# Kernel optimization log

Measured on AMD Instinct MI355X. Metric: run time of the kernel, lower is better.

Reference implementation:

```python
import jax, jax.numpy as jnp
import numpy as np

E, N, D, H = 500000, 100000, 128, 128
LN_EPS = 1e-5


def setup_inputs() -> dict:
    key = jax.random.key(0)
    ks = jax.random.split(key, 8)
    efeat = jax.random.normal(ks[0], (E, D), dtype=jnp.float32)
    nfeat = jax.random.normal(ks[1], (N, D), dtype=jnp.float32)
    src = jax.random.randint(ks[2], (E,), 0, N, dtype=jnp.int64)
    dst = jax.random.randint(ks[3], (E,), 0, N, dtype=jnp.int64)
    dim_cat = 2 * D + D  # 2*input_dim_nodes + input_dim_edges = 384
    w1 = jax.random.normal(ks[4], (dim_cat, H), dtype=jnp.float32) / np.sqrt(dim_cat)
    b1 = jnp.zeros((H,), dtype=jnp.float32)
    w2 = jax.random.normal(ks[5], (H, D), dtype=jnp.float32) / np.sqrt(H)
    b2 = jnp.zeros((D,), dtype=jnp.float32)
    gamma = jnp.ones((D,), dtype=jnp.float32)
    beta = jnp.zeros((D,), dtype=jnp.float32)
    return {"efeat": efeat, "nfeat": nfeat, "src": src, "dst": dst,
            "w1": w1, "b1": b1, "w2": w2, "b2": b2, "gamma": gamma, "beta": beta}


def reference(efeat, nfeat, src, dst, w1, b1, w2, b2, gamma, beta):
    # gather per-edge src/dst node features and concat with edge features: [E, 2D+D]
    cat_feat = jnp.concatenate([efeat, nfeat[src], nfeat[dst]], axis=-1)
    # MeshGraphMLP with hidden_layers=1: Linear -> SiLU -> Linear -> LayerNorm
    h = jax.nn.silu(cat_feat @ w1 + b1)          # [E, H]
    y = h @ w2 + b2                               # [E, D]
    mu = jnp.mean(y, axis=-1, keepdims=True)
    var = jnp.mean((y - mu) ** 2, axis=-1, keepdims=True)
    y = (y - mu) * jax.lax.rsqrt(var + LN_EPS) * gamma + beta
    efeat_new = y + efeat                         # residual add
    return (efeat_new, nfeat)
```

## Files before the change

### kernel.cpp

```cpp
#include <hip/hip_runtime.h>

#define E_CONST 500000
#define N_CONST 100000

typedef __attribute__((ext_vector_type(8))) short bf16x8;
typedef __attribute__((ext_vector_type(4))) float f32x4;
typedef __attribute__((ext_vector_type(4))) unsigned u32x4;

__global__ __launch_bounds__(256) void prep_weights(const float* __restrict__ w1,
                                                    const float* __restrict__ w2,
                                                    short* __restrict__ ws) {
    int idx  = blockIdx.x * 256 + threadIdx.x;
    int frag = idx >> 9;
    int r    = idx & 511;
    int lane = r >> 3, j = r & 7;
    const float* w;
    int fi;
    if (frag < 96) { w = w1; fi = frag; }
    else           { w = w2; fi = frag - 96; }
    int kk = fi >> 3, nn = fi & 7;
    int k = kk * 32 + (lane >> 4) * 8 + j;
    int n = nn * 16 + (lane & 15);
    unsigned u = __float_as_uint(w[k * 128 + n]);
    u = u + 0x7FFFu + ((u >> 16) & 1u);
    ws[idx] = (short)(u >> 16);
}

__global__ __launch_bounds__(256) void copy_nfeat(const float* __restrict__ nfeat,
                                                  float* __restrict__ out) {
    size_t idx = (size_t)(blockIdx.x * 256 + threadIdx.x) * 4;
    *(f32x4*)(out + idx) = *(const f32x4*)(nfeat + idx);
}

__device__ __forceinline__ unsigned pack_bf16_trunc(float lo, float hi) {
    return __builtin_amdgcn_perm(__float_as_uint(hi), __float_as_uint(lo), 0x07060302u);
}

__global__ __launch_bounds__(256, 2) void edge_mlp(
    const float* __restrict__ efeat, const float* __restrict__ nfeat,
    const int* __restrict__ src, const int* __restrict__ dst,
    const short* __restrict__ wsw,
    const float* __restrict__ b1, const float* __restrict__ b2,
    const float* __restrict__ gamma, const float* __restrict__ beta,
    float* __restrict__ out) {

    __shared__ short hs[64 * 136];
    __shared__ float ys[64 * 132];
    __shared__ float mu_s[64];
    __shared__ float rs_s[64];

    const int tid   = threadIdx.x;
    const int lane  = tid & 63;
    const int nw    = tid >> 6;
    const int l15   = lane & 15;
    const int quad  = lane >> 4;
    const int eBase = blockIdx.x * 64;

    bf16x8 b1f[2][12];
    bf16x8 b2f[2][4];
#pragma unroll
    for (int t = 0; t < 2; ++t) {
        int nn = nw * 2 + t;
#pragma unroll
        for (int kk = 0; kk < 12; ++kk)
            b1f[t][kk] = *(const bf16x8*)(wsw + ((kk * 8 + nn) * 64 + lane) * 8);
#pragma unroll
        for (int kk = 0; kk < 4; ++kk)
            b2f[t][kk] = *(const bf16x8*)(wsw + 49152 + ((kk * 8 + nn) * 64 + lane) * 8);
    }
    const float bb1[2] = { b1[nw * 32 + l15], b1[nw * 32 + 16 + l15] };
    const float bb2[2] = { b2[nw * 32 + l15], b2[nw * 32 + 16 + l15] };

#pragma unroll 1
    for (int mt = 0; mt < 4; ++mt) {
        int e = eBase + mt * 16 + l15;
        if (e >= E_CONST) e = E_CONST - 1;
        int s = src[e], d = dst[e];
        const float* pe = efeat + (size_t)e * 128 + quad * 8;
        const float* ps = nfeat + (size_t)s * 128 + quad * 8;
        const float* pd = nfeat + (size_t)d * 128 + quad * 8;

        f32x4 acc0 = {0.f, 0.f, 0.f, 0.f}, acc1 = {0.f, 0.f, 0.f, 0.f};
#pragma unroll
        for (int kk = 0; kk < 12; ++kk) {
            const float* p = (kk < 4) ? (pe + kk * 32)
                           : (kk < 8) ? (ps + (kk - 4) * 32)
                                      : (pd + (kk - 8) * 32);
            f32x4 f0 = *(const f32x4*)p;
            f32x4 f1 = *(const f32x4*)(p + 4);
            u32x4 pk;
            pk.x = pack_bf16_trunc(f0.x, f0.y);
            pk.y = pack_bf16_trunc(f0.z, f0.w);
            pk.z = pack_bf16_trunc(f1.x, f1.y);
            pk.w = pack_bf16_trunc(f1.z, f1.w);
            bf16x8 a = __builtin_bit_cast(bf16x8, pk);
            acc0 = __builtin_amdgcn_mfma_f32_16x16x32_bf16(a, b1f[0][kk], acc0, 0, 0, 0);
            acc1 = __builtin_amdgcn_mfma_f32_16x16x32_bf16(a, b1f[1][kk], acc1, 0, 0, 0);
        }
#pragma unroll
        for (int t = 0; t < 2; ++t) {
            f32x4 acc = (t == 0) ? acc0 : acc1;
            int col = nw * 32 + t * 16 + l15;
#pragma unroll
            for (int i = 0; i < 4; ++i) {
                float x  = acc[i] + bb1[t];
                float sg = __builtin_amdgcn_rcpf(1.0f + __expf(-x));
                float h  = x * sg;
                int row  = mt * 16 + quad * 4 + i;
                unsigned u = __float_as_uint(h);
                u = u + 0x7FFFu + ((u >> 16) & 1u);
                hs[row * 136 + col] = (short)(u >> 16);
            }
        }
    }
    __syncthreads();

#pragma unroll 1
    for (int mt = 0; mt < 4; ++mt) {
        int arow = mt * 16 + l15;
        f32x4 acc0 = {0.f, 0.f, 0.f, 0.f}, acc1 = {0.f, 0.f, 0.f, 0.f};
#pragma unroll
        for (int kk = 0; kk < 4; ++kk) {
            bf16x8 a = *(const bf16x8*)(hs + arow * 136 + kk * 32 + quad * 8);
            acc0 = __builtin_amdgcn_mfma_f32_16x16x32_bf16(a, b2f[0][kk], acc0, 0, 0, 0);
            acc1 = __builtin_amdgcn_mfma_f32_16x16x32_bf16(a, b2f[1][kk], acc1, 0, 0, 0);
        }
#pragma unroll
        for (int t = 0; t < 2; ++t) {
            f32x4 acc = (t == 0) ? acc0 : acc1;
            int col = nw * 32 + t * 16 + l15;
#pragma unroll
            for (int i = 0; i < 4; ++i)
                ys[(mt * 16 + quad * 4 + i) * 132 + col] = acc[i] + bb2[t];
        }
    }
    __syncthreads();

    {
        int row = tid >> 2;
        int part = tid & 3;
        const float* yr = ys + row * 132 + part * 32;
        float sum = 0.f, sq = 0.f;
#pragma unroll
        for (int k = 0; k < 8; ++k) {
            f32x4 v = *(const f32x4*)(yr + k * 4);
            sum += v.x + v.y + v.z + v.w;
            sq  += v.x * v.x + v.y * v.y + v.z * v.z + v.w * v.w;
        }
        sum += __shfl_xor(sum, 1); sq += __shfl_xor(sq, 1);
        sum += __shfl_xor(sum, 2); sq += __shfl_xor(sq, 2);
        if (part == 0) {
            float mu  = sum * (1.0f / 128.0f);
            float var = sq * (1.0f / 128.0f) - mu * mu;
            mu_s[row] = mu;
            rs_s[row] = __builtin_amdgcn_rsqf(var + 1e-5f);
        }
    }
    __syncthreads();

    {
        int c4 = tid & 31;
        f32x4 g4  = *(const f32x4*)(gamma + c4 * 4);
        f32x4 bt4 = *(const f32x4*)(beta  + c4 * 4);
#pragma unroll 1
        for (int it = 0; it < 8; ++it) {
            int row = it * 8 + (tid >> 5);
            int e = eBase + row;
            if (e < E_CONST) {
                float mu = mu_s[row], rs = rs_s[row];
                f32x4 y  = *(const f32x4*)(ys + row * 132 + c4 * 4);
                f32x4 ef = *(const f32x4*)(efeat + (size_t)e * 128 + c4 * 4);
                f32x4 o;
                o.x = (y.x - mu) * rs * g4.x + bt4.x + ef.x;
                o.y = (y.y - mu) * rs * g4.y + bt4.y + ef.y;
                o.z = (y.z - mu) * rs * g4.z + bt4.z + ef.z;
                o.w = (y.w - mu) * rs * g4.w + bt4.w + ef.w;
                *(f32x4*)(out + (size_t)e * 128 + c4 * 4) = o;
            }
        }
    }
}

extern "C" void kernel_launch(void* const* d_in, const int* in_sizes, int n_in,
                              void* d_out, int out_size, void* d_ws, size_t ws_size,
                              hipStream_t stream) {
    const float* efeat = (const float*)d_in[0];
    const float* nfeat = (const float*)d_in[1];
    const int*   src   = (const int*)d_in[2];
    const int*   dst   = (const int*)d_in[3];
    const float* w1    = (const float*)d_in[4];
    const float* b1    = (const float*)d_in[5];
    const float* w2    = (const float*)d_in[6];
    const float* b2    = (const float*)d_in[7];
    const float* gamma = (const float*)d_in[8];
    const float* beta  = (const float*)d_in[9];
    float* out = (float*)d_out;
    short* wsw = (short*)d_ws;

    hipLaunchKernelGGL(prep_weights, dim3(256), dim3(256), 0, stream, w1, w2, wsw);
    hipLaunchKernelGGL(copy_nfeat, dim3(12500), dim3(256), 0, stream,
                       nfeat, out + (size_t)E_CONST * 128);
    hipLaunchKernelGGL(edge_mlp, dim3((E_CONST + 63) / 64), dim3(256), 0, stream,
                       efeat, nfeat, src, dst, wsw, b1, b2, gamma, beta, out);
}
```

Measured before the change: 844.9 us.

## Raise occupancy by streaming weights, reusing LDS for bf16 y, batching loads

```diff
diff --git a/kernel.cpp b/kernel.cpp
--- a/kernel.cpp
+++ b/kernel.cpp
@@ -6,6 +6,8 @@
 typedef __attribute__((ext_vector_type(8))) short bf16x8;
 typedef __attribute__((ext_vector_type(4))) float f32x4;
 typedef __attribute__((ext_vector_type(4))) unsigned u32x4;
+typedef __attribute__((ext_vector_type(8))) unsigned short u16x8;
+typedef __attribute__((ext_vector_type(4))) unsigned short u16x4;
 
 __global__ __launch_bounds__(256) void prep_weights(const float* __restrict__ w1,
                                                     const float* __restrict__ w2,
@@ -26,17 +28,17 @@
     ws[idx] = (short)(u >> 16);
 }
 
-__global__ __launch_bounds__(256) void copy_nfeat(const float* __restrict__ nfeat,
-                                                  float* __restrict__ out) {
-    size_t idx = (size_t)(blockIdx.x * 256 + threadIdx.x) * 4;
-    *(f32x4*)(out + idx) = *(const f32x4*)(nfeat + idx);
-}
-
 __device__ __forceinline__ unsigned pack_bf16_trunc(float lo, float hi) {
     return __builtin_amdgcn_perm(__float_as_uint(hi), __float_as_uint(lo), 0x07060302u);
 }
 
-__global__ __launch_bounds__(256, 2) void edge_mlp(
+__device__ __forceinline__ unsigned short to_bf16(float x) {
+    unsigned u = __float_as_uint(x);
+    u = u + 0x7FFFu + ((u >> 16) & 1u);
+    return (unsigned short)(u >> 16);
+}
+
+__global__ __launch_bounds__(256, 4) void edge_mlp(
     const float* __restrict__ efeat, const float* __restrict__ nfeat,
     const int* __restrict__ src, const int* __restrict__ dst,
     const short* __restrict__ wsw,
@@ -45,7 +47,6 @@
     float* __restrict__ out) {
 
     __shared__ short hs[64 * 136];
-    __shared__ float ys[64 * 132];
     __shared__ float mu_s[64];
     __shared__ float rs_s[64];
 
@@ -56,18 +57,11 @@
     const int quad  = lane >> 4;
     const int eBase = blockIdx.x * 64;
 
-    bf16x8 b1f[2][12];
-    bf16x8 b2f[2][4];
-#pragma unroll
-    for (int t = 0; t < 2; ++t) {
-        int nn = nw * 2 + t;
-#pragma unroll
-        for (int kk = 0; kk < 12; ++kk)
-            b1f[t][kk] = *(const bf16x8*)(wsw + ((kk * 8 + nn) * 64 + lane) * 8);
-#pragma unroll
-        for (int kk = 0; kk < 4; ++kk)
-            b2f[t][kk] = *(const bf16x8*)(wsw + 49152 + ((kk * 8 + nn) * 64 + lane) * 8);
-    }
+    int ee = eBase + lane;
+    if (ee >= E_CONST) ee = E_CONST - 1;
+    const int vsrc = src[ee];
+    const int vdst = dst[ee];
+
     const float bb1[2] = { b1[nw * 32 + l15], b1[nw * 32 + 16 + l15] };
     const float bb2[2] = { b2[nw * 32 + l15], b2[nw * 32 + 16 + l15] };
 
@@ -75,27 +69,35 @@
     for (int mt = 0; mt < 4; ++mt) {
         int e = eBase + mt * 16 + l15;
         if (e >= E_CONST) e = E_CONST - 1;
-        int s = src[e], d = dst[e];
+        int s = __shfl(vsrc, mt * 16 + l15);
+        int d = __shfl(vdst, mt * 16 + l15);
         const float* pe = efeat + (size_t)e * 128 + quad * 8;
         const float* ps = nfeat + (size_t)s * 128 + quad * 8;
         const float* pd = nfeat + (size_t)d * 128 + quad * 8;
 
-        f32x4 acc0 = {0.f, 0.f, 0.f, 0.f}, acc1 = {0.f, 0.f, 0.f, 0.f};
+        f32x4 fa[12], fb[12];
 #pragma unroll
         for (int kk = 0; kk < 12; ++kk) {
             const float* p = (kk < 4) ? (pe + kk * 32)
                            : (kk < 8) ? (ps + (kk - 4) * 32)
                                       : (pd + (kk - 8) * 32);
-            f32x4 f0 = *(const f32x4*)p;
-            f32x4 f1 = *(const f32x4*)(p + 4);
+            fa[kk] = *(const f32x4*)p;
+            fb[kk] = *(const f32x4*)(p + 4);
+        }
+
+        f32x4 acc0 = {0.f, 0.f, 0.f, 0.f}, acc1 = {0.f, 0.f, 0.f, 0.f};
+#pragma unroll
+        for (int kk = 0; kk < 12; ++kk) {
             u32x4 pk;
-            pk.x = pack_bf16_trunc(f0.x, f0.y);
-            pk.y = pack_bf16_trunc(f0.z, f0.w);
-            pk.z = pack_bf16_trunc(f1.x, f1.y);
-            pk.w = pack_bf16_trunc(f1.z, f1.w);
+            pk.x = pack_bf16_trunc(fa[kk].x, fa[kk].y);
+            pk.y = pack_bf16_trunc(fa[kk].z, fa[kk].w);
+            pk.z = pack_bf16_trunc(fb[kk].x, fb[kk].y);
+            pk.w = pack_bf16_trunc(fb[kk].z, fb[kk].w);
             bf16x8 a = __builtin_bit_cast(bf16x8, pk);
-            acc0 = __builtin_amdgcn_mfma_f32_16x16x32_bf16(a, b1f[0][kk], acc0, 0, 0, 0);
-            acc1 = __builtin_amdgcn_mfma_f32_16x16x32_bf16(a, b1f[1][kk], acc1, 0, 0, 0);
+            bf16x8 w0 = *(const bf16x8*)(wsw + ((kk * 8 + nw * 2 + 0) * 64 + lane) * 8);
+            bf16x8 w1f = *(const bf16x8*)(wsw + ((kk * 8 + nw * 2 + 1) * 64 + lane) * 8);
+            acc0 = __builtin_amdgcn_mfma_f32_16x16x32_bf16(a, w0, acc0, 0, 0, 0);
+            acc1 = __builtin_amdgcn_mfma_f32_16x16x32_bf16(a, w1f, acc1, 0, 0, 0);
         }
 #pragma unroll
         for (int t = 0; t < 2; ++t) {
@@ -107,14 +109,13 @@
                 float sg = __builtin_amdgcn_rcpf(1.0f + __expf(-x));
                 float h  = x * sg;
                 int row  = mt * 16 + quad * 4 + i;
-                unsigned u = __float_as_uint(h);
-                u = u + 0x7FFFu + ((u >> 16) & 1u);
-                hs[row * 136 + col] = (short)(u >> 16);
+                hs[row * 136 + col] = (short)to_bf16(h);
             }
         }
     }
     __syncthreads();
 
+    f32x4 y0[4], y1[4];
 #pragma unroll 1
     for (int mt = 0; mt < 4; ++mt) {
         int arow = mt * 16 + l15;
@@ -122,16 +123,28 @@
 #pragma unroll
         for (int kk = 0; kk < 4; ++kk) {
             bf16x8 a = *(const bf16x8*)(hs + arow * 136 + kk * 32 + quad * 8);
-            acc0 = __builtin_amdgcn_mfma_f32_16x16x32_bf16(a, b2f[0][kk], acc0, 0, 0, 0);
-            acc1 = __builtin_amdgcn_mfma_f32_16x16x32_bf16(a, b2f[1][kk], acc1, 0, 0, 0);
-        }
-#pragma unroll
-        for (int t = 0; t < 2; ++t) {
-            f32x4 acc = (t == 0) ? acc0 : acc1;
-            int col = nw * 32 + t * 16 + l15;
-#pragma unroll
-            for (int i = 0; i < 4; ++i)
-                ys[(mt * 16 + quad * 4 + i) * 132 + col] = acc[i] + bb2[t];
+            bf16x8 w0 = *(const bf16x8*)(wsw + 49152 + ((kk * 8 + nw * 2 + 0) * 64 + lane) * 8);
+            bf16x8 w1f = *(const bf16x8*)(wsw + 49152 + ((kk * 8 + nw * 2 + 1) * 64 + lane) * 8);
+            acc0 = __builtin_amdgcn_mfma_f32_16x16x32_bf16(a, w0, acc0, 0, 0, 0);
+            acc1 = __builtin_amdgcn_mfma_f32_16x16x32_bf16(a, w1f, acc1, 0, 0, 0);
+        }
+#pragma unroll
+        for (int i = 0; i < 4; ++i) {
+            acc0[i] += bb2[0];
+            acc1[i] += bb2[1];
+        }
+        y0[mt] = acc0;
+        y1[mt] = acc1;
+    }
+    __syncthreads();
+
+#pragma unroll
+    for (int mt = 0; mt < 4; ++mt) {
+#pragma unroll
+        for (int i = 0; i < 4; ++i) {
+            int row = mt * 16 + quad * 4 + i;
+            hs[row * 136 + nw * 32 + l15]      = (short)to_bf16(y0[mt][i]);
+            hs[row * 136 + nw * 32 + 16 + l15] = (short)to_bf16(y1[mt][i]);
         }
     }
     __syncthreads();
@@ -139,13 +152,17 @@
     {
         int row = tid >> 2;
         int part = tid & 3;
-        const float* yr = ys + row * 132 + part * 32;
+        const unsigned short* yr = (const unsigned short*)hs + row * 136 + part * 32;
         float sum = 0.f, sq = 0.f;
 #pragma unroll
-        for (int k = 0; k < 8; ++k) {
-            f32x4 v = *(const f32x4*)(yr + k * 4);
-            sum += v.x + v.y + v.z + v.w;
-            sq  += v.x * v.x + v.y * v.y + v.z * v.z + v.w * v.w;
+        for (int k = 0; k < 4; ++k) {
+            u16x8 v = *(const u16x8*)(yr + k * 8);
+#pragma unroll
+            for (int j = 0; j < 8; ++j) {
+                float f = __uint_as_float((unsigned)v[j] << 16);
+                sum += f;
+                sq  += f * f;
+            }
         }
         sum += __shfl_xor(sum, 1); sq += __shfl_xor(sq, 1);
         sum += __shfl_xor(sum, 2); sq += __shfl_xor(sq, 2);
@@ -168,13 +185,13 @@
             int e = eBase + row;
             if (e < E_CONST) {
                 float mu = mu_s[row], rs = rs_s[row];
-                f32x4 y  = *(const f32x4*)(ys + row * 132 + c4 * 4);
+                u16x4 yv = *(const u16x4*)((const unsigned short*)hs + row * 136 + c4 * 4);
                 f32x4 ef = *(const f32x4*)(efeat + (size_t)e * 128 + c4 * 4);
                 f32x4 o;
-                o.x = (y.x - mu) * rs * g4.x + bt4.x + ef.x;
-                o.y = (y.y - mu) * rs * g4.y + bt4.y + ef.y;
-                o.z = (y.z - mu) * rs * g4.z + bt4.z + ef.z;
-                o.w = (y.w - mu) * rs * g4.w + bt4.w + ef.w;
+                o.x = (__uint_as_float((unsigned)yv.x << 16) - mu) * rs * g4.x + bt4.x + ef.x;
+                o.y = (__uint_as_float((unsigned)yv.y << 16) - mu) * rs * g4.y + bt4.y + ef.y;
+                o.z = (__uint_as_float((unsigned)yv.z << 16) - mu) * rs * g4.z + bt4.z + ef.z;
+                o.w = (__uint_as_float((unsigned)yv.w << 16) - mu) * rs * g4.w + bt4.w + ef.w;
                 *(f32x4*)(out + (size_t)e * 128 + c4 * 4) = o;
             }
         }
@@ -198,8 +215,9 @@
     short* wsw = (short*)d_ws;
 
     hipLaunchKernelGGL(prep_weights, dim3(256), dim3(256), 0, stream, w1, w2, wsw);
-    hipLaunchKernelGGL(copy_nfeat, dim3(12500), dim3(256), 0, stream,
-                       nfeat, out + (size_t)E_CONST * 128);
+    hipMemcpyAsync(out + (size_t)E_CONST * 128, nfeat,
+                   (size_t)N_CONST * 128 * sizeof(float),
+                   hipMemcpyDeviceToDevice, stream);
     hipLaunchKernelGGL(edge_mlp, dim3((E_CONST + 63) / 64), dim3(256), 0, stream,
                        efeat, nfeat, src, dst, wsw, b1, b2, gamma, beta, out);
 }
```

New measurement: 850.1 us. Within noise of the previous version (+0.6%).
